# Kernel optimization log

Measured on AMD Instinct MI355X. Metric: run time of the kernel, lower is better.

Reference implementation:

```python
import jax, jax.numpy as jnp
import numpy as np

EPS = 1e-5

def _layer_norm(x, w):
    mu = jnp.mean(x, axis=-1, keepdims=True)
    var = jnp.mean(jnp.square(x - mu), axis=-1, keepdims=True)
    return (x - mu) * jax.lax.rsqrt(var + EPS) * w

def setup_inputs() -> dict:
    key = jax.random.key(0)
    ks = jax.random.split(key, 5)
    B, T, C, H = 2, 2048, 1024, 16
    std = 0.02
    return {
        "x": jax.random.normal(ks[0], (B, T, C), dtype=jnp.float32),
        "ln1_w": jnp.ones((C,), dtype=jnp.float32),
        "w_attn": jax.random.normal(ks[1], (C, 3 * C), dtype=jnp.float32) * std,
        "w_proj": jax.random.normal(ks[2], (C, C), dtype=jnp.float32) * std,
        "ln2_w": jnp.ones((C,), dtype=jnp.float32),
        "w_fc": jax.random.normal(ks[3], (C, 4 * C), dtype=jnp.float32) * std,
        "w_cproj": jax.random.normal(ks[4], (4 * C, C), dtype=jnp.float32) * std,
    }

def reference(x, ln1_w, w_attn, w_proj, ln2_w, w_fc, w_cproj):
    B, T, C = x.shape
    H = 16
    Dh = C // H
    # --- causal self-attention on ln1(x) ---
    h = _layer_norm(x, ln1_w)
    qkv = h @ w_attn                      # [B,T,3C]
    q, k, v = jnp.split(qkv, 3, axis=-1)
    # [B,T,C] -> [B,H,T,Dh]
    q = q.reshape(B, T, H, Dh).transpose(0, 2, 1, 3)
    k = k.reshape(B, T, H, Dh).transpose(0, 2, 1, 3)
    v = v.reshape(B, T, H, Dh).transpose(0, 2, 1, 3)
    # NOTE: original scales by full embed dim C**-0.5, not head_dim**-0.5
    scores = jnp.einsum('bhqd,bhkd->bhqk', q, k) * (C ** -0.5)
    causal = jnp.tril(jnp.ones((T, T), dtype=bool))
    scores = jnp.where(causal, scores, -jnp.inf)
    probs = jax.nn.softmax(scores, axis=-1)  # dropout=0.0 (eval)
    y = jnp.einsum('bhqk,bhkd->bhqd', probs, v)
    y = y.transpose(0, 2, 1, 3).reshape(B, T, C)
    x = x + y @ w_proj
    # --- MLP on ln2(x) ---
    h = _layer_norm(x, ln2_w)
    x = x + jax.nn.relu(h @ w_fc) @ w_cproj
    return x
```

## Files before the change

kernel.cpp:

```cpp
#include <hip/hip_runtime.h>

typedef __attribute__((ext_vector_type(8))) __bf16 bf16x8;
typedef __attribute__((ext_vector_type(4))) float f32x4;
typedef __attribute__((ext_vector_type(8))) unsigned short u16x8;
typedef unsigned short u16;

__device__ __forceinline__ u16 f2bf(float f) {
  return __builtin_bit_cast(u16, (__bf16)f);
}
__device__ __forceinline__ float bf2f(u16 u) {
  return __builtin_bit_cast(float, ((unsigned)u) << 16);
}

__device__ __forceinline__ f32x4 mfma16(bf16x8 a, bf16x8 b, f32x4 c) {
  return __builtin_amdgcn_mfma_f32_16x16x32_bf16(a, b, c, 0, 0, 0);
}

__device__ __forceinline__ void gl_lds16(const void* g, void* l) {
  __builtin_amdgcn_global_load_lds(
      (const __attribute__((address_space(1))) unsigned int*)g,
      (__attribute__((address_space(3))) unsigned int*)l, 16, 0, 0);
}

__global__ __launch_bounds__(256) void convT(const float* __restrict__ in,
                                             u16* __restrict__ outT, int K, int N) {
  __shared__ float tile[64][65];
  const int t = threadIdx.x;
  const int tk = blockIdx.x * 64, tn = blockIdx.y * 64;
  const int lk = t >> 4, ln = (t & 15) * 4;
#pragma unroll
  for (int r = 0; r < 4; ++r) {
    const int k = lk + r * 16;
    const float4 v = *(const float4*)(in + (size_t)(tk + k) * N + tn + ln);
    tile[k][ln + 0] = v.x; tile[k][ln + 1] = v.y;
    tile[k][ln + 2] = v.z; tile[k][ln + 3] = v.w;
  }
  __syncthreads();
  const int sn = t >> 2, sk = (t & 3) * 4;
#pragma unroll
  for (int j = 0; j < 4; ++j) {
    const int k = sk + j * 16;
    ushort4 o;
    o.x = f2bf(tile[k + 0][sn]); o.y = f2bf(tile[k + 1][sn]);
    o.z = f2bf(tile[k + 2][sn]); o.w = f2bf(tile[k + 3][sn]);
    *(ushort4*)(outT + (size_t)(tn + sn) * K + tk + k) = o;
  }
}

__global__ __launch_bounds__(256) void ln_bf16(const float* __restrict__ x,
                                               const float* __restrict__ wgt,
                                               u16* __restrict__ out) {
  const int row = blockIdx.x, t = threadIdx.x;
  const float4 v = ((const float4*)(x + (size_t)row * 1024))[t];
  float s = v.x + v.y + v.z + v.w;
  float q = v.x * v.x + v.y * v.y + v.z * v.z + v.w * v.w;
#pragma unroll
  for (int d = 32; d; d >>= 1) { s += __shfl_xor(s, d); q += __shfl_xor(q, d); }
  __shared__ float sb[8];
  const int wv = t >> 6;
  if ((t & 63) == 0) { sb[wv] = s; sb[4 + wv] = q; }
  __syncthreads();
  s = sb[0] + sb[1] + sb[2] + sb[3];
  q = sb[4] + sb[5] + sb[6] + sb[7];
  const float mu = s * (1.f / 1024.f);
  const float rstd = rsqrtf(q * (1.f / 1024.f) - mu * mu + 1e-5f);
  const float4 w4 = ((const float4*)wgt)[t];
  ushort4 o;
  o.x = f2bf((v.x - mu) * rstd * w4.x);
  o.y = f2bf((v.y - mu) * rstd * w4.y);
  o.z = f2bf((v.z - mu) * rstd * w4.z);
  o.w = f2bf((v.w - mu) * rstd * w4.w);
  *(ushort4*)(out + (size_t)row * 1024 + t * 4) = o;
}

__global__ __launch_bounds__(256) void reduce_ln(const float* __restrict__ x,
                                                 const u16* __restrict__ p, int nseg,
                                                 const float* __restrict__ wgt,
                                                 float* __restrict__ x1,
                                                 u16* __restrict__ h2) {
  const int row = blockIdx.x, t = threadIdx.x;
  const size_t ro = (size_t)row * 1024 + t * 4;
  float4 v = *(const float4*)(x + ro);
  for (int sgm = 0; sgm < nseg; ++sgm) {
    const ushort4 u = *(const ushort4*)(p + (size_t)sgm * 4096 * 1024 + ro);
    v.x += bf2f(u.x); v.y += bf2f(u.y); v.z += bf2f(u.z); v.w += bf2f(u.w);
  }
  *(float4*)(x1 + ro) = v;
  float s = v.x + v.y + v.z + v.w;
  float q = v.x * v.x + v.y * v.y + v.z * v.z + v.w * v.w;
#pragma unroll
  for (int d = 32; d; d >>= 1) { s += __shfl_xor(s, d); q += __shfl_xor(q, d); }
  __shared__ float sb[8];
  const int wv = t >> 6;
  if ((t & 63) == 0) { sb[wv] = s; sb[4 + wv] = q; }
  __syncthreads();
  s = sb[0] + sb[1] + sb[2] + sb[3];
  q = sb[4] + sb[5] + sb[6] + sb[7];
  const float mu = s * (1.f / 1024.f);
  const float rstd = rsqrtf(q * (1.f / 1024.f) - mu * mu + 1e-5f);
  const float4 w4 = ((const float4*)wgt)[t];
  ushort4 o;
  o.x = f2bf((v.x - mu) * rstd * w4.x);
  o.y = f2bf((v.y - mu) * rstd * w4.y);
  o.z = f2bf((v.z - mu) * rstd * w4.z);
  o.w = f2bf((v.w - mu) * rstd * w4.w);
  *(ushort4*)(h2 + ro) = o;
}

__global__ __launch_bounds__(256) void reduce_out(const float* __restrict__ x1,
                                                  const u16* __restrict__ p, int nseg,
                                                  float* __restrict__ out) {
  const int i = blockIdx.x * blockDim.x + threadIdx.x;
  const size_t ro = (size_t)i * 4;
  float4 v = *(const float4*)(x1 + ro);
  for (int sgm = 0; sgm < nseg; ++sgm) {
    const ushort4 u = *(const ushort4*)(p + (size_t)sgm * 4096 * 1024 + ro);
    v.x += bf2f(u.x); v.y += bf2f(u.y); v.z += bf2f(u.z); v.w += bf2f(u.w);
  }
  *(float4*)(out + ro) = v;
}

template <int EPI>
__global__ __launch_bounds__(256) void gemm128(const u16* __restrict__ A,
                                               const u16* __restrict__ Bt,
                                               void* __restrict__ outp,
                                               int M, int N, int K) {
  __shared__ u16 As[2][4096];
  __shared__ u16 Bs[2][4096];
  const unsigned gx = gridDim.x, gy = gridDim.y, gxy = gx * gy;
  const unsigned nwg = gxy * gridDim.z;
  unsigned f = (blockIdx.z * gy + blockIdx.y) * gx + blockIdx.x;
  if ((nwg & 7u) == 0u) { const unsigned qq = nwg >> 3; f = (f & 7u) * qq + (f >> 3); }
  const int bx = f % gx, by = (f / gx) % gy, bz = f / gxy;

  const int t = threadIdx.x, w = t >> 6, l = t & 63;
  const int lr = l & 15, g = l >> 4;
  const int row0 = by * 128, col0 = bx * 128;
  const int segK = K / gridDim.z;
  const int k0 = bz * segK, kend = k0 + segK;
  const int wr = w >> 1, wc = w & 1;
  f32x4 acc[4][4] = {};

  const int sr = t >> 2;
  const int sk = (t & 3) << 3;
  const u16* Ag = A + (size_t)(row0 + sr) * K + sk;
  const u16* Bg = Bt + (size_t)(col0 + sr) * K + sk;
  const size_t rstride = (size_t)64 * K;

  auto stage = [&](int kt, int bb) {
    u16* AsW = As[bb] + w * 512;
    u16* BsW = Bs[bb] + w * 512;
    gl_lds16(Ag + kt, AsW);
    gl_lds16(Ag + kt + rstride, AsW + 2048);
    gl_lds16(Bg + kt, BsW);
    gl_lds16(Bg + kt + rstride, BsW + 2048);
  };

  stage(k0, 0);
  __syncthreads();
  int cur = 0;
  for (int kt = k0; kt < kend; kt += 32) {
    if (kt + 32 < kend) stage(kt + 32, cur ^ 1);
    bf16x8 af[4], bfr[4];
#pragma unroll
    for (int m = 0; m < 4; ++m)
      af[m] = *(const bf16x8*)(As[cur] + (wr * 64 + m * 16 + lr) * 32 + g * 8);
#pragma unroll
    for (int n = 0; n < 4; ++n)
      bfr[n] = *(const bf16x8*)(Bs[cur] + (wc * 64 + n * 16 + lr) * 32 + g * 8);
#pragma unroll
    for (int m = 0; m < 4; ++m)
#pragma unroll
      for (int n = 0; n < 4; ++n) acc[m][n] = mfma16(af[m], bfr[n], acc[m][n]);
    __syncthreads();
    cur ^= 1;
  }

  const size_t segoff = (size_t)bz * M * N;
#pragma unroll
  for (int m = 0; m < 4; ++m)
#pragma unroll
    for (int n = 0; n < 4; ++n)
#pragma unroll
      for (int r = 0; r < 4; ++r) {
        const int row = row0 + wr * 64 + m * 16 + g * 4 + r;
        const int col = col0 + wc * 64 + n * 16 + lr;
        const size_t idx = (size_t)row * N + col;
        const float v = acc[m][n][r];
        if constexpr (EPI == 0) ((u16*)outp)[idx] = f2bf(v);
        else if constexpr (EPI == 2) ((u16*)outp)[idx] = f2bf(fmaxf(v, 0.f));
        else ((u16*)outp)[segoff + idx] = f2bf(v);
      }
}

__global__ __launch_bounds__(256) void attn_fwd(const u16* __restrict__ qkvb,
                                                u16* __restrict__ y) {
  __shared__ u16 Ks[2][4096];
  __shared__ u16 Vt[2][64 * 80];
  __shared__ u16 Pb[4][16 * 72];
  const int t = threadIdx.x, w = t >> 6, l = t & 63;
  const int lr = l & 15, g = l >> 4;
  const unsigned f = blockIdx.y * gridDim.x + blockIdx.x;
  const int xcd = f & 7, j = f >> 3;
  const int bh = xcd + 8 * (j & 3);
  const int qt = 31 - (j >> 2);
  const int b = bh >> 4, h = bh & 15;
  const size_t base = (size_t)b * 2048 * 3072;
  const u16* Kg = qkvb + base + 1024 + h * 64;
  const u16* Vg = qkvb + base + 2048 + h * 64;
  u16* Pw = &Pb[w][0];
  const int vkv = t & 63;
  const int vd0 = (t >> 6) * 16;

  auto stageK = [&](int kv0, int bb) {
#pragma unroll
    for (int r = 0; r < 2; ++r) {
      const int dl = (r * 256 + t) * 16;
      const int row = dl >> 7;
      const int srcb = (dl & 127) ^ ((row & 7) << 4);
      gl_lds16(Kg + (size_t)(kv0 + row) * 3072 + (srcb >> 1),
               (char*)Ks[bb] + r * 4096 + w * 1024);
    }
  };

  const int q0 = qt * 64, q0w = q0 + w * 16, nt = qt + 1;
  const u16* Qp = qkvb + base + (size_t)(q0w + lr) * 3072 + h * 64;
  const bf16x8 qf0 = *(const bf16x8*)(Qp + g * 8);
  const bf16x8 qf1 = *(const bf16x8*)(Qp + 32 + g * 8);
  f32x4 o[4] = {};
  float m_run[4] = {-1e30f, -1e30f, -1e30f, -1e30f};
  float s_lane[4] = {0.f, 0.f, 0.f, 0.f};

  stageK(0, 0);
  u16x8 v0 = *(const u16x8*)(Vg + (size_t)vkv * 3072 + vd0);
  u16x8 v1 = *(const u16x8*)(Vg + (size_t)vkv * 3072 + vd0 + 8);
#pragma unroll
  for (int jj = 0; jj < 8; ++jj) {
    Vt[0][(vd0 + jj) * 80 + vkv] = v0[jj];
    Vt[0][(vd0 + 8 + jj) * 80 + vkv] = v1[jj];
  }
  __syncthreads();

  int ct = 0;
  for (int tt = 0; tt < nt; ++tt) {
    const int kv0 = tt * 64;
    const bool more = (tt + 1 < nt);
    if (more) {
      stageK(kv0 + 64, ct ^ 1);
      v0 = *(const u16x8*)(Vg + (size_t)(kv0 + 64 + vkv) * 3072 + vd0);
      v1 = *(const u16x8*)(Vg + (size_t)(kv0 + 64 + vkv) * 3072 + vd0 + 8);
    }

    const u16* Kbuf = Ks[ct];
    f32x4 s4[4];
#pragma unroll
    for (int i = 0; i < 4; ++i) {
      const int row = i * 16 + lr;
      const int sw = (row & 7) << 4;
      const bf16x8 k0 = *(const bf16x8*)(Kbuf + row * 64 + (((g * 16) ^ sw) >> 1));
      const bf16x8 k1 = *(const bf16x8*)(Kbuf + row * 64 + (((64 + g * 16) ^ sw) >> 1));
      f32x4 z = {0.f, 0.f, 0.f, 0.f};
      z = mfma16(qf0, k0, z);
      z = mfma16(qf1, k1, z);
      s4[i] = z * 0.03125f;
    }
    if (kv0 + 64 > q0w) {
#pragma unroll
      for (int i = 0; i < 4; ++i) {
        const int col = kv0 + i * 16 + lr;
#pragma unroll
        for (int r = 0; r < 4; ++r)
          if (col > q0w + g * 4 + r) s4[i][r] = -1e30f;
      }
    }
#pragma unroll
    for (int r = 0; r < 4; ++r) {
      float mx = fmaxf(fmaxf(s4[0][r], s4[1][r]), fmaxf(s4[2][r], s4[3][r]));
      mx = fmaxf(mx, __shfl_xor(mx, 1));
      mx = fmaxf(mx, __shfl_xor(mx, 2));
      mx = fmaxf(mx, __shfl_xor(mx, 4));
      mx = fmaxf(mx, __shfl_xor(mx, 8));
      const float mnew = fmaxf(m_run[r], mx);
      const float sc = __expf(m_run[r] - mnew);
      m_run[r] = mnew;
      const float p0 = __expf(s4[0][r] - mnew), p1 = __expf(s4[1][r] - mnew);
      const float p2 = __expf(s4[2][r] - mnew), p3 = __expf(s4[3][r] - mnew);
      s_lane[r] = s_lane[r] * sc + (p0 + p1) + (p2 + p3);
      o[0][r] *= sc; o[1][r] *= sc; o[2][r] *= sc; o[3][r] *= sc;
      const int pr = (g * 4 + r) * 72 + lr;
      Pw[pr] = f2bf(p0); Pw[pr + 16] = f2bf(p1);
      Pw[pr + 32] = f2bf(p2); Pw[pr + 48] = f2bf(p3);
    }
#pragma unroll
    for (int s = 0; s < 2; ++s) {
      const bf16x8 pa = *(const bf16x8*)(Pw + lr * 72 + s * 32 + g * 8);
#pragma unroll
      for (int n = 0; n < 4; ++n) {
        const bf16x8 vf =
            *(const bf16x8*)(&Vt[ct][(n * 16 + lr) * 80 + s * 32 + g * 8]);
        o[n] = mfma16(pa, vf, o[n]);
      }
    }
    if (more) {
#pragma unroll
      for (int jj = 0; jj < 8; ++jj) {
        Vt[ct ^ 1][(vd0 + jj) * 80 + vkv] = v0[jj];
        Vt[ct ^ 1][(vd0 + 8 + jj) * 80 + vkv] = v1[jj];
      }
    }
    __syncthreads();
    ct ^= 1;
  }

  float inv[4];
#pragma unroll
  for (int r = 0; r < 4; ++r) {
    float den = s_lane[r];
    den += __shfl_xor(den, 1);
    den += __shfl_xor(den, 2);
    den += __shfl_xor(den, 4);
    den += __shfl_xor(den, 8);
    inv[r] = 1.f / den;
  }
#pragma unroll
  for (int n = 0; n < 4; ++n)
#pragma unroll
    for (int r = 0; r < 4; ++r) {
      const int row = q0w + g * 4 + r;
      const int col = h * 64 + n * 16 + lr;
      y[(size_t)(b * 2048 + row) * 1024 + col] = f2bf(o[n][r] * inv[r]);
    }
}

extern "C" void kernel_launch(void* const* d_in, const int* in_sizes, int n_in,
                              void* d_out, int out_size, void* d_ws, size_t ws_size,
                              hipStream_t stream) {
  const float* x      = (const float*)d_in[0];
  const float* ln1w   = (const float*)d_in[1];
  const float* wattn  = (const float*)d_in[2];
  const float* wproj  = (const float*)d_in[3];
  const float* ln2w   = (const float*)d_in[4];
  const float* wfc    = (const float*)d_in[5];
  const float* wcproj = (const float*)d_in[6];
  float* out = (float*)d_out;
  char* ws = (char*)d_ws;
  const size_t MB = 1024 * 1024;
  u16* qkvb    = (u16*)(ws + 0);
  u16* cprojP  = (u16*)(ws + 0);
  u16* h1      = (u16*)(ws + 24 * MB);
  u16* yb      = (u16*)(ws + 24 * MB);
  u16* projP   = (u16*)(ws + 32 * MB);
  float* x1    = (float*)(ws + 48 * MB);
  u16* h2      = (u16*)(ws + 64 * MB);
  u16* hf      = (u16*)(ws + 72 * MB);
  u16* wattnT  = (u16*)(ws + 104 * MB);
  u16* wprojT  = (u16*)(ws + 110 * MB);
  u16* wcprojT = (u16*)(ws + 104 * MB);
  u16* wfcT    = (u16*)(ws + 112 * MB);

  convT<<<dim3(16, 48), 256, 0, stream>>>(wattn, wattnT, 1024, 3072);
  convT<<<dim3(16, 16), 256, 0, stream>>>(wproj, wprojT, 1024, 1024);
  convT<<<dim3(16, 64), 256, 0, stream>>>(wfc, wfcT, 1024, 4096);

  ln_bf16<<<4096, 256, 0, stream>>>(x, ln1w, h1);
  gemm128<0><<<dim3(24, 32, 1), 256, 0, stream>>>(h1, wattnT, qkvb, 4096, 3072, 1024);
  attn_fwd<<<dim3(32, 32), 256, 0, stream>>>(qkvb, yb);
  gemm128<4><<<dim3(8, 32, 2), 256, 0, stream>>>(yb, wprojT, projP, 4096, 1024, 1024);
  convT<<<dim3(64, 16), 256, 0, stream>>>(wcproj, wcprojT, 4096, 1024);
  reduce_ln<<<4096, 256, 0, stream>>>(x, projP, 2, ln2w, x1, h2);
  gemm128<2><<<dim3(32, 32, 1), 256, 0, stream>>>(h2, wfcT, hf, 4096, 4096, 1024);
  gemm128<4><<<dim3(8, 32, 4), 256, 0, stream>>>(hf, wcprojT, cprojP, 4096, 1024, 4096);
  reduce_out<<<4096, 256, 0, stream>>>(x1, cprojP, 4, out);
}
```

Measured before the change: 266.3 us.

## Transpose QK^T MFMA, use exp2 with lazy max rescaling in attention

```diff
diff --git a/kernel.cpp b/kernel.cpp
--- a/kernel.cpp
+++ b/kernel.cpp
@@ -3,6 +3,7 @@
 typedef __attribute__((ext_vector_type(8))) __bf16 bf16x8;
 typedef __attribute__((ext_vector_type(4))) float f32x4;
 typedef __attribute__((ext_vector_type(8))) unsigned short u16x8;
+typedef __attribute__((ext_vector_type(4))) unsigned short u16x4;
 typedef unsigned short u16;
 
 __device__ __forceinline__ u16 f2bf(float f) {
@@ -20,6 +21,13 @@
   __builtin_amdgcn_global_load_lds(
       (const __attribute__((address_space(1))) unsigned int*)g,
       (__attribute__((address_space(3))) unsigned int*)l, 16, 0, 0);
+}
+
+__device__ __forceinline__ f32x4 fmax4(f32x4 a, f32x4 b) {
+  f32x4 r;
+  r[0] = fmaxf(a[0], b[0]); r[1] = fmaxf(a[1], b[1]);
+  r[2] = fmaxf(a[2], b[2]); r[3] = fmaxf(a[3], b[3]);
+  return r;
 }
 
 __global__ __launch_bounds__(256) void convT(const float* __restrict__ in,
@@ -196,7 +204,7 @@
 __global__ __launch_bounds__(256) void attn_fwd(const u16* __restrict__ qkvb,
                                                 u16* __restrict__ y) {
   __shared__ u16 Ks[2][4096];
-  __shared__ u16 Vt[2][64 * 80];
+  __shared__ u16 Vt[64 * 80];
   __shared__ u16 Pb[4][16 * 72];
   const int t = threadIdx.x, w = t >> 6, l = t & 63;
   const int lr = l & 15, g = l >> 4;
@@ -211,6 +219,7 @@
   u16* Pw = &Pb[w][0];
   const int vkv = t & 63;
   const int vd0 = (t >> 6) * 16;
+  const float SCL = 0.0450842200277855f;
 
   auto stageK = [&](int kv0, int bb) {
 #pragma unroll
@@ -228,16 +237,15 @@
   const bf16x8 qf0 = *(const bf16x8*)(Qp + g * 8);
   const bf16x8 qf1 = *(const bf16x8*)(Qp + 32 + g * 8);
   f32x4 o[4] = {};
-  float m_run[4] = {-1e30f, -1e30f, -1e30f, -1e30f};
-  float s_lane[4] = {0.f, 0.f, 0.f, 0.f};
+  float m1 = -1e30f, s1 = 0.f;
 
   stageK(0, 0);
   u16x8 v0 = *(const u16x8*)(Vg + (size_t)vkv * 3072 + vd0);
   u16x8 v1 = *(const u16x8*)(Vg + (size_t)vkv * 3072 + vd0 + 8);
 #pragma unroll
   for (int jj = 0; jj < 8; ++jj) {
-    Vt[0][(vd0 + jj) * 80 + vkv] = v0[jj];
-    Vt[0][(vd0 + 8 + jj) * 80 + vkv] = v1[jj];
+    Vt[(vd0 + jj) * 80 + vkv] = v0[jj];
+    Vt[(vd0 + 8 + jj) * 80 + vkv] = v1[jj];
   }
   __syncthreads();
 
@@ -260,75 +268,82 @@
       const bf16x8 k0 = *(const bf16x8*)(Kbuf + row * 64 + (((g * 16) ^ sw) >> 1));
       const bf16x8 k1 = *(const bf16x8*)(Kbuf + row * 64 + (((64 + g * 16) ^ sw) >> 1));
       f32x4 z = {0.f, 0.f, 0.f, 0.f};
-      z = mfma16(qf0, k0, z);
-      z = mfma16(qf1, k1, z);
-      s4[i] = z * 0.03125f;
+      z = mfma16(k0, qf0, z);
+      z = mfma16(k1, qf1, z);
+      s4[i] = z * SCL;
     }
     if (kv0 + 64 > q0w) {
 #pragma unroll
-      for (int i = 0; i < 4; ++i) {
-        const int col = kv0 + i * 16 + lr;
+      for (int i = 0; i < 4; ++i)
 #pragma unroll
         for (int r = 0; r < 4; ++r)
-          if (col > q0w + g * 4 + r) s4[i][r] = -1e30f;
+          if (kv0 + i * 16 + g * 4 + r > q0w + lr) s4[i][r] = -1e30f;
+    }
+    const f32x4 mm = fmax4(fmax4(s4[0], s4[1]), fmax4(s4[2], s4[3]));
+    float mx = fmaxf(fmaxf(mm[0], mm[1]), fmaxf(mm[2], mm[3]));
+    mx = fmaxf(mx, __shfl_xor(mx, 16));
+    mx = fmaxf(mx, __shfl_xor(mx, 32));
+    if (!__all(mx <= m1 + 8.f)) {
+      const float mn = fmaxf(m1, mx);
+      const float sc = exp2f(m1 - mn);
+      m1 = mn;
+      s1 *= sc;
+      float scr[4];
+#pragma unroll
+      for (int r = 0; r < 4; ++r) scr[r] = __shfl(sc, g * 4 + r);
+#pragma unroll
+      for (int n = 0; n < 4; ++n)
+#pragma unroll
+        for (int r = 0; r < 4; ++r) o[n][r] *= scr[r];
+    }
+    float ps = 0.f;
+#pragma unroll
+    for (int i = 0; i < 4; ++i) {
+      u16x4 pk;
+#pragma unroll
+      for (int r = 0; r < 4; ++r) {
+        const float p = exp2f(s4[i][r] - m1);
+        ps += p;
+        pk[r] = f2bf(p);
       }
-    }
-#pragma unroll
-    for (int r = 0; r < 4; ++r) {
-      float mx = fmaxf(fmaxf(s4[0][r], s4[1][r]), fmaxf(s4[2][r], s4[3][r]));
-      mx = fmaxf(mx, __shfl_xor(mx, 1));
-      mx = fmaxf(mx, __shfl_xor(mx, 2));
-      mx = fmaxf(mx, __shfl_xor(mx, 4));
-      mx = fmaxf(mx, __shfl_xor(mx, 8));
-      const float mnew = fmaxf(m_run[r], mx);
-      const float sc = __expf(m_run[r] - mnew);
-      m_run[r] = mnew;
-      const float p0 = __expf(s4[0][r] - mnew), p1 = __expf(s4[1][r] - mnew);
-      const float p2 = __expf(s4[2][r] - mnew), p3 = __expf(s4[3][r] - mnew);
-      s_lane[r] = s_lane[r] * sc + (p0 + p1) + (p2 + p3);
-      o[0][r] *= sc; o[1][r] *= sc; o[2][r] *= sc; o[3][r] *= sc;
-      const int pr = (g * 4 + r) * 72 + lr;
-      Pw[pr] = f2bf(p0); Pw[pr + 16] = f2bf(p1);
-      Pw[pr + 32] = f2bf(p2); Pw[pr + 48] = f2bf(p3);
-    }
+      *(u16x4*)(Pw + lr * 72 + i * 16 + g * 4) = pk;
+    }
+    s1 += ps;
 #pragma unroll
     for (int s = 0; s < 2; ++s) {
       const bf16x8 pa = *(const bf16x8*)(Pw + lr * 72 + s * 32 + g * 8);
 #pragma unroll
       for (int n = 0; n < 4; ++n) {
-        const bf16x8 vf =
-            *(const bf16x8*)(&Vt[ct][(n * 16 + lr) * 80 + s * 32 + g * 8]);
+        const bf16x8 vf = *(const bf16x8*)(&Vt[(n * 16 + lr) * 80 + s * 32 + g * 8]);
         o[n] = mfma16(pa, vf, o[n]);
       }
     }
+    __syncthreads();
     if (more) {
 #pragma unroll
       for (int jj = 0; jj < 8; ++jj) {
-        Vt[ct ^ 1][(vd0 + jj) * 80 + vkv] = v0[jj];
-        Vt[ct ^ 1][(vd0 + 8 + jj) * 80 + vkv] = v1[jj];
+        Vt[(vd0 + jj) * 80 + vkv] = v0[jj];
+        Vt[(vd0 + 8 + jj) * 80 + vkv] = v1[jj];
       }
     }
     __syncthreads();
     ct ^= 1;
   }
 
-  float inv[4];
-#pragma unroll
-  for (int r = 0; r < 4; ++r) {
-    float den = s_lane[r];
-    den += __shfl_xor(den, 1);
-    den += __shfl_xor(den, 2);
-    den += __shfl_xor(den, 4);
-    den += __shfl_xor(den, 8);
-    inv[r] = 1.f / den;
-  }
+  float den = s1;
+  den += __shfl_xor(den, 16);
+  den += __shfl_xor(den, 32);
+  const float iv = 1.f / den;
+  float ivr[4];
+#pragma unroll
+  for (int r = 0; r < 4; ++r) ivr[r] = __shfl(iv, g * 4 + r);
 #pragma unroll
   for (int n = 0; n < 4; ++n)
 #pragma unroll
     for (int r = 0; r < 4; ++r) {
       const int row = q0w + g * 4 + r;
       const int col = h * 64 + n * 16 + lr;
-      y[(size_t)(b * 2048 + row) * 1024 + col] = f2bf(o[n][r] * inv[r]);
+      y[(size_t)(b * 2048 + row) * 1024 + col] = f2bf(o[n][r] * ivr[r]);
     }
 }
 
```

New measurement: 258.7 us. 2.9% less time.
